# Kernel tuning notes

Measured on AMD Instinct MI355X. Metric: run time of the kernel, lower is better.

Reference implementation:

```python
import jax, jax.numpy as jnp
import numpy as np

NUM_LAYER = 5
EMB = 300
FEAT = 512
NUM_GRAPHS = 64
BN_EPS = 1e-5


def setup_inputs() -> dict:
    key = jax.random.key(0)
    ks = jax.random.split(key, 32)
    N, E = 16000, 256000
    x = jax.random.randint(ks[0], (N, 2), 0, 3)  # col0: atom type (<119), col1: chirality (<3)
    edge_index = jax.random.randint(ks[1], (2, E), 0, N)
    edge_attr = jax.random.randint(ks[2], (E, 2), 0, 3)  # col0: bond type (<6), col1: direction (<3)
    batch = jnp.sort(jax.random.randint(ks[3], (N,), 0, NUM_GRAPHS))

    def xav(k, shape):
        fan_in, fan_out = shape[-2], shape[-1]
        lim = float(np.sqrt(6.0 / (fan_in + fan_out)))
        return jax.random.uniform(k, shape, jnp.float32, -lim, lim)

    inp = dict(x=x, edge_index=edge_index, edge_attr=edge_attr, batch=batch)
    inp['x_emb1'] = xav(ks[4], (119, EMB))
    inp['x_emb2'] = xav(ks[5], (3, EMB))
    inp['e1_emb'] = xav(ks[6], (NUM_LAYER, 6, EMB))
    inp['e2_emb'] = xav(ks[7], (NUM_LAYER, 3, EMB))
    inp['w1'] = xav(ks[8], (NUM_LAYER, EMB, 2 * EMB))
    inp['b1'] = jnp.zeros((NUM_LAYER, 2 * EMB))
    inp['w2'] = xav(ks[9], (NUM_LAYER, 2 * EMB, EMB))
    inp['b2'] = jnp.zeros((NUM_LAYER, EMB))
    inp['bn_g'] = jnp.ones((NUM_LAYER, EMB))
    inp['bn_b'] = jnp.zeros((NUM_LAYER, EMB))
    inp['feat_w'] = xav(ks[10], (EMB, FEAT))
    inp['feat_b'] = jnp.zeros((FEAT,))
    inp['hw1'] = xav(ks[11], (FEAT, FEAT // 2))
    inp['hb1'] = jnp.zeros((FEAT // 2,))
    inp['hw2'] = xav(ks[12], (FEAT // 2, FEAT // 2))
    inp['hb2'] = jnp.zeros((FEAT // 2,))
    inp['hw3'] = xav(ks[13], (FEAT // 2, 2))
    inp['hb3'] = jnp.zeros((2,))
    return inp


def gin_forward(x, edge_index, edge_attr, batch,
                x_emb1, x_emb2, e1_emb, e2_emb, w1, b1, w2, b2,
                bn_g, bn_b, feat_w, feat_b, hw1, hb1, hw2, hb2, hw3, hb3):
    N = x.shape[0]
    h = x_emb1[x[:, 0]] + x_emb2[x[:, 1]]  # [N, EMB]
    # add self-loops once (same for every layer): attr = (5, 0)
    loops = jnp.broadcast_to(jnp.arange(N)[None, :], (2, N))
    ei = jnp.concatenate([edge_index, loops], axis=1)  # [2, E+N]
    loop_attr = jnp.concatenate([jnp.full((N, 1), 5, edge_attr.dtype),
                                 jnp.zeros((N, 1), edge_attr.dtype)], axis=1)
    ea = jnp.concatenate([edge_attr, loop_attr], axis=0)  # [E+N, 2]
    src, dst = ei[0], ei[1]
    for l in range(NUM_LAYER):
        edge_emb = e1_emb[l][ea[:, 0]] + e2_emb[l][ea[:, 1]]  # [E+N, EMB]
        msg = h[src] + edge_emb
        agg = jax.ops.segment_sum(msg, dst, num_segments=N)  # scatter-add
        h = jax.nn.relu(agg @ w1[l] + b1[l]) @ w2[l] + b2[l]  # GIN MLP update
        mean = jnp.mean(h, axis=0)
        var = jnp.var(h, axis=0)
        h = (h - mean) * jax.lax.rsqrt(var + BN_EPS) * bn_g[l] + bn_b[l]
        if l < NUM_LAYER - 1:
            h = jax.nn.relu(h)
    # global mean pool per graph
    sums = jax.ops.segment_sum(h, batch, num_segments=NUM_GRAPHS)
    cnts = jax.ops.segment_sum(jnp.ones((N,), h.dtype), batch, num_segments=NUM_GRAPHS)
    hg = sums / jnp.maximum(cnts, 1.0)[:, None]  # [G, EMB]
    hf = hg @ feat_w + feat_b  # [G, FEAT]
    p = jax.nn.softplus(hf @ hw1 + hb1)
    p = jax.nn.softplus(p @ hw2 + hb2)
    pred = p @ hw3 + hb3  # [G, 2]
    return hf, pred


def reference(x, edge_index, edge_attr, batch,
              x_emb1, x_emb2, e1_emb, e2_emb, w1, b1, w2, b2,
              bn_g, bn_b, feat_w, feat_b, hw1, hb1, hw2, hb2, hw3, hb3):
    return gin_forward(x, edge_index, edge_attr, batch,
                       x_emb1, x_emb2, e1_emb, e2_emb, w1, b1, w2, b2,
                       bn_g, bn_b, feat_w, feat_b, hw1, hb1, hw2, hb2, hw3, hb3)
```

## Files before the change

### kernel.cpp

```cpp
#include <hip/hip_runtime.h>

#define NODES 16000
#define EDGES 256000
#define EMB   300
#define KP1   320
#define NP1   640
#define NP2B  384
#define NGRAPH 64
#define LAYERS 5
#define INV_N (1.0f / 16000.0f)

typedef unsigned short u16;
typedef unsigned int u32;
typedef __bf16 bf16_t;
typedef bf16_t bf16x8 __attribute__((ext_vector_type(8)));
typedef float f32x4 __attribute__((ext_vector_type(4)));

__device__ inline u16 f2bf(float f) {
    bf16_t b = (bf16_t)f;
    return __builtin_bit_cast(u16, b);
}
__device__ inline float bf_lo(u32 u) { return __builtin_bit_cast(float, u << 16); }
__device__ inline float bf_hi(u32 u) { return __builtin_bit_cast(float, u & 0xFFFF0000u); }
__device__ inline u32 bf_pack(float lo, float hi) {
    return ((u32)f2bf(hi) << 16) | (u32)f2bf(lo);
}

__device__ inline float softplus_f(float x) {
    return fmaxf(x, 0.f) + log1pf(expf(-fabsf(x)));
}

__device__ inline void gload_lds16(const u16* g, u16* l) {
    __builtin_amdgcn_global_load_lds(
        (const __attribute__((address_space(1))) void*)g,
        (__attribute__((address_space(3))) void*)l, 16, 0, 0);
}

__device__ inline void bn_coef_v(float ss, float qq, float gg, float bb,
                                 float& s, float& t) {
    float mean = ss * INV_N;
    float var = qq * INV_N - mean * mean;
    float rstd = rsqrtf(var + 1e-5f);
    s = rstd * gg;
    t = bb - mean * s;
}

__global__ void k_count(const int* __restrict__ ei, int* __restrict__ cnt) {
    int e = blockIdx.x * 256 + threadIdx.x;
    if (e >= EDGES) return;
    atomicAdd(&cnt[ei[EDGES + e]], 1);
}

__global__ __launch_bounds__(1024) void k_scan(const int* __restrict__ cnt,
                                               int* __restrict__ row_off,
                                               int* __restrict__ cursor) {
    __shared__ int wsum[16];
    int t = threadIdx.x;
    int lane = t & 63, w = t >> 6;
    int base = t * 16;
    int pre[16];
    int run = 0;
#pragma unroll
    for (int i = 0; i < 16; ++i) {
        int idx = base + i;
        int v = (idx < NODES) ? cnt[idx] : 0;
        pre[i] = run;
        run += v;
    }
    int inc = run;
#pragma unroll
    for (int off = 1; off < 64; off <<= 1) {
        int n = __shfl_up(inc, off);
        if (lane >= off) inc += n;
    }
    if (lane == 63) wsum[w] = inc;
    __syncthreads();
    int wpre = 0;
    for (int i = 0; i < w; ++i) wpre += wsum[i];
    int excl = wpre + inc - run;
#pragma unroll
    for (int i = 0; i < 16; ++i) {
        int idx = base + i;
        if (idx < NODES) {
            int st = excl + pre[i];
            row_off[idx] = st;
            cursor[idx] = st;
        }
    }
    if (t == 1023) row_off[NODES] = wpre + inc;
}

__global__ void k_fill(const int* __restrict__ ei, const int* __restrict__ ea,
                       int* __restrict__ cursor, int* __restrict__ packed) {
    int e = blockIdx.x * 256 + threadIdx.x;
    if (e >= EDGES) return;
    int src = ei[e];
    int dst = ei[EDGES + e];
    int c = ea[e * 2] * 3 + ea[e * 2 + 1];
    int pos = atomicAdd(&cursor[dst], 1);
    packed[pos] = src | (c << 20);
}

#define SEG0 1200000
#define SEG1 6750
#define SEG2 256000
#define SEG3 307200
#define SETUP_TOT (SEG0 + SEG1 + SEG2 + SEG3 + NGRAPH + 1)

__global__ __launch_bounds__(256) void k_setup(
    const int* __restrict__ x, const float* __restrict__ e1x,
    const float* __restrict__ e2x, const float* __restrict__ ce1,
    const float* __restrict__ ce2, const float* __restrict__ w1,
    const float* __restrict__ w2, const int* __restrict__ batch,
    u16* __restrict__ h, u16* __restrict__ comb,
    u16* __restrict__ w1bT, u16* __restrict__ w2bT, int* __restrict__ goff) {
    int id = blockIdx.x * 256 + threadIdx.x;
    if (id < SEG0) {
        int base = id * 4;
        int row = base / EMB;
        int f = base - row * EMB;
        int x1 = x[2 * row], x2 = x[2 * row + 1];
        float4 a = *(const float4*)(e1x + x1 * EMB + f);
        float4 b = *(const float4*)(e2x + x2 * EMB + f);
        u32* o = (u32*)h + id * 2;
        o[0] = bf_pack(a.x + b.x, a.y + b.y);
        o[1] = bf_pack(a.z + b.z, a.w + b.w);
        return;
    }
    id -= SEG0;
    if (id < SEG1) {
        int l = id / 1350, r = id - l * 1350;
        int c = r / 75, f = (r - c * 75) * 4;
        int a = c / 3, bb = c - a * 3;
        float4 va = *(const float4*)(ce1 + (l * 6 + a) * EMB + f);
        float4 vb = *(const float4*)(ce2 + (l * 3 + bb) * EMB + f);
        u32* o = (u32*)comb + ((l * 18 + c) * EMB + f) / 2;
        o[0] = bf_pack(va.x + vb.x, va.y + vb.y);
        o[1] = bf_pack(va.z + vb.z, va.w + vb.w);
        return;
    }
    id -= SEG1;
    if (id < SEG2) {
        int l = id / (NP1 * 80), r = id - l * (NP1 * 80);
        int n = r / 80, k4 = (r - n * 80) * 4;
        float v[4];
#pragma unroll
        for (int j = 0; j < 4; ++j) {
            int k = k4 + j;
            v[j] = (n < 600 && k < EMB) ? w1[(l * EMB + k) * 600 + n] : 0.f;
        }
        u32* o = (u32*)w1bT + ((size_t)(l * NP1 + n) * KP1 + k4) / 2;
        o[0] = bf_pack(v[0], v[1]);
        o[1] = bf_pack(v[2], v[3]);
        return;
    }
    id -= SEG2;
    if (id < SEG3) {
        int l = id / (NP2B * 160), r = id - l * (NP2B * 160);
        int n = r / 160, k4 = (r - n * 160) * 4;
        float v[4];
#pragma unroll
        for (int j = 0; j < 4; ++j) {
            int k = k4 + j;
            v[j] = (n < EMB && k < 600) ? w2[(l * 600 + k) * EMB + n] : 0.f;
        }
        u32* o = (u32*)w2bT + ((size_t)(l * NP2B + n) * NP1 + k4) / 2;
        o[0] = bf_pack(v[0], v[1]);
        o[1] = bf_pack(v[2], v[3]);
        return;
    }
    id -= SEG3;
    if (id <= NGRAPH) {
        int lo = 0, hi = NODES;
        while (lo < hi) { int mid = (lo + hi) >> 1; if (batch[mid] < id) lo = mid + 1; else hi = mid; }
        goff[id] = lo;
    }
}

__global__ __launch_bounds__(256) void k_bnrelu(
    const u16* __restrict__ hin, u16* __restrict__ hout,
    const float* __restrict__ ssum, const float* __restrict__ ssq,
    const float* __restrict__ g, const float* __restrict__ b) {
    int id = blockIdx.x * 256 + threadIdx.x;
    if (id >= NODES * EMB / 4) return;
    int base = id * 4;
    int row = base / EMB;
    int f = base - row * EMB;
    float4 S = *(const float4*)(ssum + f);
    float4 Q = *(const float4*)(ssq + f);
    float4 G = *(const float4*)(g + f);
    float4 B = *(const float4*)(b + f);
    const u32* in = (const u32*)hin + id * 2;
    u32 x0 = in[0], x1 = in[1];
    float sc0, tc0, sc1, tc1, sc2, tc2, sc3, tc3;
    bn_coef_v(S.x, Q.x, G.x, B.x, sc0, tc0);
    bn_coef_v(S.y, Q.y, G.y, B.y, sc1, tc1);
    bn_coef_v(S.z, Q.z, G.z, B.z, sc2, tc2);
    bn_coef_v(S.w, Q.w, G.w, B.w, sc3, tc3);
    float v0 = fmaxf(bf_lo(x0) * sc0 + tc0, 0.f);
    float v1 = fmaxf(bf_hi(x0) * sc1 + tc1, 0.f);
    float v2 = fmaxf(bf_lo(x1) * sc2 + tc2, 0.f);
    float v3 = fmaxf(bf_hi(x1) * sc3 + tc3, 0.f);
    u32* o = (u32*)hout + id * 2;
    o[0] = bf_pack(v0, v1);
    o[1] = bf_pack(v2, v3);
}

#define AGG_E(Q)                                                \
    {                                                           \
        const u32* hr = hu + (size_t)((Q) & 0xFFFFF) * 150;     \
        const u32* cr = cu + ((Q) >> 20) * 150;                 \
        u32 u0 = hr[lane], u1 = hr[64 + lane];                  \
        u32 v0 = cr[lane], v1 = cr[64 + lane];                  \
        u32 u2 = 0, v2 = 0;                                     \
        if (has2) { u2 = hr[128 + lane]; v2 = cr[128 + lane]; } \
        a0l += bf_lo(u0) + bf_lo(v0);                           \
        a0h += bf_hi(u0) + bf_hi(v0);                           \
        a1l += bf_lo(u1) + bf_lo(v1);                           \
        a1h += bf_hi(u1) + bf_hi(v1);                           \
        a2l += bf_lo(u2) + bf_lo(v2);                           \
        a2h += bf_hi(u2) + bf_hi(v2);                           \
    }

__global__ __launch_bounds__(256) void k_aggregate(
    const u16* __restrict__ h, const int* __restrict__ row_off,
    const int* __restrict__ packed, const u16* __restrict__ comb,
    u16* __restrict__ aggB) {
    int node = blockIdx.x * 4 + (threadIdx.x >> 6);
    int lane = threadIdx.x & 63;
    int s = row_off[node], e = row_off[node + 1];
    bool has2 = lane < 22;
    const u32* hu = (const u32*)h;
    const u32* cu = (const u32*)comb;
    float a0l = 0, a0h = 0, a1l = 0, a1h = 0, a2l = 0, a2h = 0;
    {
        const u32* hr = hu + (size_t)node * 150;
        const u32* cr = cu + 15 * 150;
        u32 u0 = hr[lane], u1 = hr[64 + lane];
        u32 v0 = cr[lane], v1 = cr[64 + lane];
        u32 u2 = 0, v2 = 0;
        if (has2) { u2 = hr[128 + lane]; v2 = cr[128 + lane]; }
        a0l = bf_lo(u0) + bf_lo(v0);
        a0h = bf_hi(u0) + bf_hi(v0);
        a1l = bf_lo(u1) + bf_lo(v1);
        a1h = bf_hi(u1) + bf_hi(v1);
        a2l = bf_lo(u2) + bf_lo(v2);
        a2h = bf_hi(u2) + bf_hi(v2);
    }
    int p = s;
    for (; p + 3 < e; p += 4) {
        int q0 = __builtin_amdgcn_readfirstlane(packed[p]);
        int q1 = __builtin_amdgcn_readfirstlane(packed[p + 1]);
        int q2 = __builtin_amdgcn_readfirstlane(packed[p + 2]);
        int q3 = __builtin_amdgcn_readfirstlane(packed[p + 3]);
        AGG_E(q0); AGG_E(q1); AGG_E(q2); AGG_E(q3);
    }
    for (; p < e; ++p) {
        int q = __builtin_amdgcn_readfirstlane(packed[p]);
        AGG_E(q);
    }
    u32* o = (u32*)(aggB + (size_t)node * KP1);
    o[lane] = bf_pack(a0l, a0h);
    o[64 + lane] = bf_pack(a1l, a1h);
    if (lane < 32) o[128 + lane] = has2 ? bf_pack(a2l, a2h) : 0u;
}

template <int MODE>
__global__ __launch_bounds__(256) void k_gemm(
    const u16* __restrict__ A, const u16* __restrict__ Bt,
    const float* __restrict__ bias, int nbias,
    u16* __restrict__ Cv, int ldc, int K,
    float* __restrict__ ssum, float* __restrict__ ssq) {
    __shared__ __align__(16) u16 Al[128 * 32];
    __shared__ __align__(16) u16 Bl[128 * 32];
    __shared__ float rs[2][128];
    __shared__ float rq[2][128];
    int t = threadIdx.x;
    int n0 = blockIdx.x * 128, m0 = blockIdx.y * 128;
    int lane = t & 63, w = t >> 6;
    int wr = w >> 1, wc = w & 1;
    int lr = lane >> 2, lc = lane & 3;
    const u16* gA0 = A + (size_t)(m0 + w * 32 + lr) * K + lc * 8;
    const u16* gA1 = gA0 + (size_t)16 * K;
    const u16* gB0 = Bt + (size_t)(n0 + w * 32 + lr) * K + lc * 8;
    const u16* gB1 = gB0 + (size_t)16 * K;
    u16* lA0 = &Al[(w * 32) * 32];
    u16* lA1 = &Al[(w * 32 + 16) * 32];
    u16* lB0 = &Bl[(w * 32) * 32];
    u16* lB1 = &Bl[(w * 32 + 16) * 32];
    f32x4 acc[4][4];
#pragma unroll
    for (int i = 0; i < 4; i++)
#pragma unroll
        for (int j = 0; j < 4; j++) acc[i][j] = (f32x4){0.f, 0.f, 0.f, 0.f};
    int fr = lane & 15;
    int k0 = (lane >> 4) * 8;
    int abase = (wr * 64 + fr) * 32 + k0;
    int bbase = (wc * 64 + fr) * 32 + k0;
    for (int kt = 0; kt < K; kt += 32) {
        if (kt) __syncthreads();
        gload_lds16(gA0 + kt, lA0);
        gload_lds16(gA1 + kt, lA1);
        gload_lds16(gB0 + kt, lB0);
        gload_lds16(gB1 + kt, lB1);
        __syncthreads();
        bf16x8 af[4], bfv[4];
#pragma unroll
        for (int f = 0; f < 4; ++f) {
            af[f]  = *reinterpret_cast<const bf16x8*>(&Al[abase + f * 16 * 32]);
            bfv[f] = *reinterpret_cast<const bf16x8*>(&Bl[bbase + f * 16 * 32]);
        }
#pragma unroll
        for (int fm = 0; fm < 4; ++fm)
#pragma unroll
            for (int fn = 0; fn < 4; ++fn)
                acc[fm][fn] = __builtin_amdgcn_mfma_f32_16x16x32_bf16(
                    af[fm], bfv[fn], acc[fm][fn], 0, 0, 0);
    }
    int rg = lane >> 4;
    if (MODE == 0) {
#pragma unroll
        for (int fn = 0; fn < 4; ++fn) {
            int col = n0 + wc * 64 + fn * 16 + fr;
            float bv = (col < nbias) ? bias[col] : 0.f;
#pragma unroll
            for (int fm = 0; fm < 4; ++fm) {
                int rb = m0 + wr * 64 + fm * 16 + rg * 4;
#pragma unroll
                for (int j = 0; j < 4; ++j) {
                    float v = fmaxf(acc[fm][fn][j] + bv, 0.f);
                    Cv[(size_t)(rb + j) * ldc + col] = f2bf(v);
                }
            }
        }
    } else {
#pragma unroll
        for (int fn = 0; fn < 4; ++fn) {
            int col = n0 + wc * 64 + fn * 16 + fr;
            float bv = (col < nbias) ? bias[col] : 0.f;
            float cs = 0.f, cq = 0.f;
#pragma unroll
            for (int fm = 0; fm < 4; ++fm) {
                int rb = m0 + wr * 64 + fm * 16 + rg * 4;
#pragma unroll
                for (int j = 0; j < 4; ++j) {
                    float v = acc[fm][fn][j] + bv;
                    if (col < EMB) Cv[(size_t)(rb + j) * EMB + col] = f2bf(v);
                    cs += v;
                    cq += v * v;
                }
            }
            cs += __shfl_xor(cs, 16); cs += __shfl_xor(cs, 32);
            cq += __shfl_xor(cq, 16); cq += __shfl_xor(cq, 32);
            if (rg == 0) {
                rs[wr][wc * 64 + fn * 16 + fr] = cs;
                rq[wr][wc * 64 + fn * 16 + fr] = cq;
            }
        }
        __syncthreads();
        if (t < 128) {
            int col = n0 + t;
            if (col < EMB) {
                atomicAdd(&ssum[col], rs[0][t] + rs[1][t]);
                atomicAdd(&ssq[col], rq[0][t] + rq[1][t]);
            }
        }
    }
}

__global__ __launch_bounds__(256) void k_pool(const u16* __restrict__ h,
                                              const int* __restrict__ goff,
                                              const float* __restrict__ ssum,
                                              const float* __restrict__ ssq,
                                              const float* __restrict__ bng,
                                              const float* __restrict__ bnb,
                                              float* __restrict__ hg) {
    __shared__ float red[4][64];
    int g = blockIdx.x;
    int col = blockIdx.y * 64 + (threadIdx.x & 63);
    int w = threadIdx.x >> 6;
    int s = goff[g], e = goff[g + 1];
    float a = 0.f;
    bool ok = col < EMB;
    if (ok) {
        for (int r = s + w; r < e; r += 4)
            a += __builtin_bit_cast(float, (u32)h[(size_t)r * EMB + col] << 16);
    }
    red[w][threadIdx.x & 63] = a;
    __syncthreads();
    if (w == 0 && ok) {
        float sc, tc;
        bn_coef_v(ssum[col], ssq[col], bng[col], bnb[col], sc, tc);
        float v = red[0][threadIdx.x] + red[1][threadIdx.x] +
                  red[2][threadIdx.x] + red[3][threadIdx.x];
        float inv = (e > s) ? 1.0f / (float)(e - s) : 0.f;
        hg[(size_t)g * EMB + col] = (v * inv) * sc + tc;
    }
}

template <int ACT>
__global__ __launch_bounds__(256) void k_small_mm(
    const float* __restrict__ A, const float* __restrict__ W,
    const float* __restrict__ bias, float* __restrict__ C, int N, int K) {
    __shared__ float red[4][64];
    int row = blockIdx.x;
    int lane = threadIdx.x & 63;
    int col = blockIdx.y * 64 + lane;
    int w = threadIdx.x >> 6;
    const float* a = A + (size_t)row * K;
    float acc = 0.f;
#pragma unroll 4
    for (int k = w; k < K; k += 4) acc += a[k] * W[(size_t)k * N + col];
    red[w][lane] = acc;
    __syncthreads();
    if (w == 0) {
        float v = red[0][lane] + red[1][lane] + red[2][lane] + red[3][lane] + bias[col];
        if (ACT) v = softplus_f(v);
        C[(size_t)row * N + col] = v;
    }
}

__global__ __launch_bounds__(256) void k_pred(const float* __restrict__ P,
                                              const float* __restrict__ hw3,
                                              const float* __restrict__ hb3,
                                              float* __restrict__ out) {
    __shared__ float red[2][4];
    int g = blockIdx.x;
    int t = threadIdx.x;
    float q = P[(size_t)g * 256 + t];
    float r0 = q * hw3[t * 2 + 0];
    float r1 = q * hw3[t * 2 + 1];
#pragma unroll
    for (int off = 32; off > 0; off >>= 1) {
        r0 += __shfl_down(r0, off);
        r1 += __shfl_down(r1, off);
    }
    if ((t & 63) == 0) { red[0][t >> 6] = r0; red[1][t >> 6] = r1; }
    __syncthreads();
    if (t == 0) {
        out[(size_t)NGRAPH * 512 + g * 2 + 0] = red[0][0] + red[0][1] + red[0][2] + red[0][3] + hb3[0];
        out[(size_t)NGRAPH * 512 + g * 2 + 1] = red[1][0] + red[1][1] + red[1][2] + red[1][3] + hb3[1];
    }
}

extern "C" void kernel_launch(void* const* d_in, const int* in_sizes, int n_in,
                              void* d_out, int out_size, void* d_ws, size_t ws_size,
                              hipStream_t stream) {
    const int* x      = (const int*)d_in[0];
    const int* ei     = (const int*)d_in[1];
    const int* ea     = (const int*)d_in[2];
    const int* batch  = (const int*)d_in[3];
    const float* x_emb1 = (const float*)d_in[4];
    const float* x_emb2 = (const float*)d_in[5];
    const float* e1_emb = (const float*)d_in[6];
    const float* e2_emb = (const float*)d_in[7];
    const float* w1   = (const float*)d_in[8];
    const float* b1   = (const float*)d_in[9];
    const float* w2   = (const float*)d_in[10];
    const float* b2   = (const float*)d_in[11];
    const float* bn_g = (const float*)d_in[12];
    const float* bn_b = (const float*)d_in[13];
    const float* feat_w = (const float*)d_in[14];
    const float* feat_b = (const float*)d_in[15];
    const float* hw1  = (const float*)d_in[16];
    const float* hb1  = (const float*)d_in[17];
    const float* hw2  = (const float*)d_in[18];
    const float* hb2  = (const float*)d_in[19];
    const float* hw3  = (const float*)d_in[20];
    const float* hb3  = (const float*)d_in[21];
    float* out = (float*)d_out;

    char* p = (char*)d_ws;
    auto alloc = [&](size_t bytes) -> char* {
        char* r = p;
        p += ((bytes + 255) / 256) * 256;
        return r;
    };
    u16* h_a     = (u16*)alloc((size_t)NODES * EMB * 2);
    u16* h_b     = (u16*)alloc((size_t)NODES * EMB * 2);
    u16* aggB    = (u16*)alloc((size_t)NODES * KP1 * 2);
    u16* T       = (u16*)alloc((size_t)NODES * NP1 * 2);
    u16* w1bT    = (u16*)alloc((size_t)LAYERS * NP1 * KP1 * 2);
    u16* w2bT    = (u16*)alloc((size_t)LAYERS * NP2B * NP1 * 2);
    u16* comb    = (u16*)alloc((size_t)LAYERS * 18 * EMB * 2);
    int* row_off = (int*)alloc((NODES + 1) * 4);
    int* packed  = (int*)alloc((size_t)EDGES * 4);
    int* goff    = (int*)alloc((NGRAPH + 1) * 4);
    float* hg    = (float*)alloc((size_t)NGRAPH * EMB * 4);
    float* pb1   = (float*)alloc((size_t)NGRAPH * 256 * 4);
    float* pb2   = (float*)alloc((size_t)NGRAPH * 256 * 4);
    int* cursor  = (int*)alloc(NODES * 4);
    float* stats5 = (float*)alloc((size_t)LAYERS * 640 * 4);
    if ((size_t)(p - (char*)d_ws) > ws_size) return;

    hipMemsetAsync(cursor, 0, NODES * 4 + LAYERS * 640 * 4, stream);

    k_count<<<(EDGES + 255) / 256, 256, 0, stream>>>(ei, cursor);
    k_scan<<<1, 1024, 0, stream>>>(cursor, row_off, cursor);
    k_fill<<<(EDGES + 255) / 256, 256, 0, stream>>>(ei, ea, cursor, packed);

    k_setup<<<(SETUP_TOT + 255) / 256, 256, 0, stream>>>(
        x, x_emb1, x_emb2, e1_emb, e2_emb, w1, w2, batch,
        h_a, comb, w1bT, w2bT, goff);

    for (int l = 0; l < LAYERS; ++l) {
        const u16* h_src;
        if (l == 0) {
            h_src = h_a;
        } else {
            float* st = stats5 + (size_t)(l - 1) * 640;
            k_bnrelu<<<(NODES * EMB / 4 + 255) / 256, 256, 0, stream>>>(
                h_a, h_b, st, st + 320, bn_g + (l - 1) * EMB, bn_b + (l - 1) * EMB);
            h_src = h_b;
        }
        k_aggregate<<<NODES / 4, 256, 0, stream>>>(
            h_src, row_off, packed, comb + (size_t)l * 18 * EMB, aggB);
        k_gemm<0><<<dim3(NP1 / 128, NODES / 128), 256, 0, stream>>>(
            aggB, w1bT + (size_t)l * NP1 * KP1, b1 + l * 600, 600, T, NP1, KP1,
            nullptr, nullptr);
        float* st = stats5 + (size_t)l * 640;
        k_gemm<1><<<dim3(NP2B / 128, NODES / 128), 256, 0, stream>>>(
            T, w2bT + (size_t)l * NP2B * NP1, b2 + l * EMB, EMB, h_a, 0, NP1,
            st, st + 320);
    }

    float* st4 = stats5 + (size_t)4 * 640;
    k_pool<<<dim3(NGRAPH, 5), 256, 0, stream>>>(h_a, goff, st4, st4 + 320,
                                                bn_g + 4 * EMB, bn_b + 4 * EMB, hg);
    k_small_mm<0><<<dim3(NGRAPH, 8), 256, 0, stream>>>(hg, feat_w, feat_b, out, 512, EMB);
    k_small_mm<1><<<dim3(NGRAPH, 4), 256, 0, stream>>>(out, hw1, hb1, pb1, 256, 512);
    k_small_mm<1><<<dim3(NGRAPH, 4), 256, 0, stream>>>(pb1, hw2, hb2, pb2, 256, 256);
    k_pred<<<NGRAPH, 256, 0, stream>>>(pb2, hw3, hb3, out);
}
```

Measured before the change: 463.7 us.

## Factor edge-embedding sums into per-node bond-type counts in aggregation

k_fill now also builds a per-node histogram over the 18 edge-attribute combos. k_aggregate then gathers only neighbour features per edge and adds each combo embedding once, scaled by its count, instead of loading a combo row for every edge. The feature gathers and the output store also use 8-byte vector loads and stores. This roughly halves the per-edge global reads, at the cost of an extra atomic per edge in setup and 18 count reads per node.

```diff
diff --git a/kernel.cpp b/kernel.cpp
--- a/kernel.cpp
+++ b/kernel.cpp
@@ -91,7 +91,8 @@
 }
 
 __global__ void k_fill(const int* __restrict__ ei, const int* __restrict__ ea,
-                       int* __restrict__ cursor, int* __restrict__ packed) {
+                       int* __restrict__ cursor, int* __restrict__ packed,
+                       int* __restrict__ cnt18) {
     int e = blockIdx.x * 256 + threadIdx.x;
     if (e >= EDGES) return;
     int src = ei[e];
@@ -99,6 +100,7 @@
     int c = ea[e * 2] * 3 + ea[e * 2 + 1];
     int pos = atomicAdd(&cursor[dst], 1);
     packed[pos] = src | (c << 20);
+    atomicAdd(&cnt18[dst * 18 + c], 1);
 }
 
 #define SEG0 1200000
@@ -209,23 +211,18 @@
 #define AGG_E(Q)                                                \
     {                                                           \
         const u32* hr = hu + (size_t)((Q) & 0xFFFFF) * 150;     \
-        const u32* cr = cu + ((Q) >> 20) * 150;                 \
-        u32 u0 = hr[lane], u1 = hr[64 + lane];                  \
-        u32 v0 = cr[lane], v1 = cr[64 + lane];                  \
-        u32 u2 = 0, v2 = 0;                                     \
-        if (has2) { u2 = hr[128 + lane]; v2 = cr[128 + lane]; } \
-        a0l += bf_lo(u0) + bf_lo(v0);                           \
-        a0h += bf_hi(u0) + bf_hi(v0);                           \
-        a1l += bf_lo(u1) + bf_lo(v1);                           \
-        a1h += bf_hi(u1) + bf_hi(v1);                           \
-        a2l += bf_lo(u2) + bf_lo(v2);                           \
-        a2h += bf_hi(u2) + bf_hi(v2);                           \
+        uint2 u01 = *(const uint2*)(hr + 2 * lane);             \
+        u32 u2 = 0;                                             \
+        if (has2) u2 = hr[128 + lane];                          \
+        a0l += bf_lo(u01.x); a0h += bf_hi(u01.x);               \
+        a1l += bf_lo(u01.y); a1h += bf_hi(u01.y);               \
+        a2l += bf_lo(u2);    a2h += bf_hi(u2);                  \
     }
 
 __global__ __launch_bounds__(256) void k_aggregate(
     const u16* __restrict__ h, const int* __restrict__ row_off,
     const int* __restrict__ packed, const u16* __restrict__ comb,
-    u16* __restrict__ aggB) {
+    const int* __restrict__ cnt18, u16* __restrict__ aggB) {
     int node = blockIdx.x * 4 + (threadIdx.x >> 6);
     int lane = threadIdx.x & 63;
     int s = row_off[node], e = row_off[node + 1];
@@ -235,17 +232,12 @@
     float a0l = 0, a0h = 0, a1l = 0, a1h = 0, a2l = 0, a2h = 0;
     {
         const u32* hr = hu + (size_t)node * 150;
-        const u32* cr = cu + 15 * 150;
-        u32 u0 = hr[lane], u1 = hr[64 + lane];
-        u32 v0 = cr[lane], v1 = cr[64 + lane];
-        u32 u2 = 0, v2 = 0;
-        if (has2) { u2 = hr[128 + lane]; v2 = cr[128 + lane]; }
-        a0l = bf_lo(u0) + bf_lo(v0);
-        a0h = bf_hi(u0) + bf_hi(v0);
-        a1l = bf_lo(u1) + bf_lo(v1);
-        a1h = bf_hi(u1) + bf_hi(v1);
-        a2l = bf_lo(u2) + bf_lo(v2);
-        a2h = bf_hi(u2) + bf_hi(v2);
+        uint2 u01 = *(const uint2*)(hr + 2 * lane);
+        u32 u2 = 0;
+        if (has2) u2 = hr[128 + lane];
+        a0l = bf_lo(u01.x); a0h = bf_hi(u01.x);
+        a1l = bf_lo(u01.y); a1h = bf_hi(u01.y);
+        a2l = bf_lo(u2);    a2h = bf_hi(u2);
     }
     int p = s;
     for (; p + 3 < e; p += 4) {
@@ -259,9 +251,26 @@
         int q = __builtin_amdgcn_readfirstlane(packed[p]);
         AGG_E(q);
     }
+    const int* cb = cnt18 + node * 18;
+#pragma unroll
+    for (int c = 0; c < 18; ++c) {
+        int cv = cb[c] + (c == 15 ? 1 : 0);
+        if (cv) {
+            float fc = (float)cv;
+            const u32* cr = cu + c * 150;
+            uint2 v01 = *(const uint2*)(cr + 2 * lane);
+            u32 v2 = 0;
+            if (has2) v2 = cr[128 + lane];
+            a0l += fc * bf_lo(v01.x); a0h += fc * bf_hi(v01.x);
+            a1l += fc * bf_lo(v01.y); a1h += fc * bf_hi(v01.y);
+            a2l += fc * bf_lo(v2);    a2h += fc * bf_hi(v2);
+        }
+    }
     u32* o = (u32*)(aggB + (size_t)node * KP1);
-    o[lane] = bf_pack(a0l, a0h);
-    o[64 + lane] = bf_pack(a1l, a1h);
+    uint2 w01;
+    w01.x = bf_pack(a0l, a0h);
+    w01.y = bf_pack(a1l, a1h);
+    *(uint2*)(o + 2 * lane) = w01;
     if (lane < 32) o[128 + lane] = has2 ? bf_pack(a2l, a2h) : 0u;
 }
 
@@ -489,15 +498,17 @@
     float* hg    = (float*)alloc((size_t)NGRAPH * EMB * 4);
     float* pb1   = (float*)alloc((size_t)NGRAPH * 256 * 4);
     float* pb2   = (float*)alloc((size_t)NGRAPH * 256 * 4);
-    int* cursor  = (int*)alloc(NODES * 4);
+    int* cursor   = (int*)alloc(NODES * 4);
     float* stats5 = (float*)alloc((size_t)LAYERS * 640 * 4);
+    int* cnt18    = (int*)alloc((size_t)NODES * 18 * 4);
     if ((size_t)(p - (char*)d_ws) > ws_size) return;
 
-    hipMemsetAsync(cursor, 0, NODES * 4 + LAYERS * 640 * 4, stream);
+    hipMemsetAsync(cursor, 0, NODES * 4 + LAYERS * 640 * 4 + (size_t)NODES * 18 * 4,
+                   stream);
 
     k_count<<<(EDGES + 255) / 256, 256, 0, stream>>>(ei, cursor);
     k_scan<<<1, 1024, 0, stream>>>(cursor, row_off, cursor);
-    k_fill<<<(EDGES + 255) / 256, 256, 0, stream>>>(ei, ea, cursor, packed);
+    k_fill<<<(EDGES + 255) / 256, 256, 0, stream>>>(ei, ea, cursor, packed, cnt18);
 
     k_setup<<<(SETUP_TOT + 255) / 256, 256, 0, stream>>>(
         x, x_emb1, x_emb2, e1_emb, e2_emb, w1, w2, batch,
@@ -514,7 +525,7 @@
             h_src = h_b;
         }
         k_aggregate<<<NODES / 4, 256, 0, stream>>>(
-            h_src, row_off, packed, comb + (size_t)l * 18 * EMB, aggB);
+            h_src, row_off, packed, comb + (size_t)l * 18 * EMB, cnt18, aggB);
         k_gemm<0><<<dim3(NP1 / 128, NODES / 128), 256, 0, stream>>>(
             aggB, w1bT + (size_t)l * NP1 * KP1, b1 + l * 600, 600, T, NP1, KP1,
             nullptr, nullptr);
```

After: 519.8 us. +12.1%, slower.

## Double-buffer LDS tiles in GEMM to overlap global loads with MFMA

Applied to the files above, without the earlier changes.

Splits the GEMM's A and B shared-memory tiles into two buffers. The next K-slice is prefetched with direct-to-LDS loads while the current slice feeds the MFMA instructions, and one barrier per step replaces two. This aims to hide global load latency behind compute, at the cost of doubled LDS use per block, which may lower occupancy. Correctness depends on the barrier also covering completion of the async LDS loads (vmcnt) before the buffer is read.

```diff
diff --git a/kernel.cpp b/kernel.cpp
--- a/kernel.cpp
+++ b/kernel.cpp
@@ -271,8 +271,8 @@
     const float* __restrict__ bias, int nbias,
     u16* __restrict__ Cv, int ldc, int K,
     float* __restrict__ ssum, float* __restrict__ ssq) {
-    __shared__ __align__(16) u16 Al[128 * 32];
-    __shared__ __align__(16) u16 Bl[128 * 32];
+    __shared__ __align__(16) u16 Al[2][128 * 32];
+    __shared__ __align__(16) u16 Bl[2][128 * 32];
     __shared__ float rs[2][128];
     __shared__ float rq[2][128];
     int t = threadIdx.x;
@@ -284,10 +284,8 @@
     const u16* gA1 = gA0 + (size_t)16 * K;
     const u16* gB0 = Bt + (size_t)(n0 + w * 32 + lr) * K + lc * 8;
     const u16* gB1 = gB0 + (size_t)16 * K;
-    u16* lA0 = &Al[(w * 32) * 32];
-    u16* lA1 = &Al[(w * 32 + 16) * 32];
-    u16* lB0 = &Bl[(w * 32) * 32];
-    u16* lB1 = &Bl[(w * 32 + 16) * 32];
+    int lds0 = (w * 32) * 32;
+    int lds1 = (w * 32 + 16) * 32;
     f32x4 acc[4][4];
 #pragma unroll
     for (int i = 0; i < 4; i++)
@@ -297,18 +295,26 @@
     int k0 = (lane >> 4) * 8;
     int abase = (wr * 64 + fr) * 32 + k0;
     int bbase = (wc * 64 + fr) * 32 + k0;
-    for (int kt = 0; kt < K; kt += 32) {
-        if (kt) __syncthreads();
-        gload_lds16(gA0 + kt, lA0);
-        gload_lds16(gA1 + kt, lA1);
-        gload_lds16(gB0 + kt, lB0);
-        gload_lds16(gB1 + kt, lB1);
-        __syncthreads();
+    int nsteps = K >> 5;
+    gload_lds16(gA0, &Al[0][lds0]);
+    gload_lds16(gA1, &Al[0][lds1]);
+    gload_lds16(gB0, &Bl[0][lds0]);
+    gload_lds16(gB1, &Bl[0][lds1]);
+    __syncthreads();
+    int cur = 0;
+    for (int s = 0; s < nsteps; ++s) {
+        if (s + 1 < nsteps) {
+            int kt = (s + 1) << 5;
+            gload_lds16(gA0 + kt, &Al[cur ^ 1][lds0]);
+            gload_lds16(gA1 + kt, &Al[cur ^ 1][lds1]);
+            gload_lds16(gB0 + kt, &Bl[cur ^ 1][lds0]);
+            gload_lds16(gB1 + kt, &Bl[cur ^ 1][lds1]);
+        }
         bf16x8 af[4], bfv[4];
 #pragma unroll
         for (int f = 0; f < 4; ++f) {
-            af[f]  = *reinterpret_cast<const bf16x8*>(&Al[abase + f * 16 * 32]);
-            bfv[f] = *reinterpret_cast<const bf16x8*>(&Bl[bbase + f * 16 * 32]);
+            af[f]  = *reinterpret_cast<const bf16x8*>(&Al[cur][abase + f * 16 * 32]);
+            bfv[f] = *reinterpret_cast<const bf16x8*>(&Bl[cur][bbase + f * 16 * 32]);
         }
 #pragma unroll
         for (int fm = 0; fm < 4; ++fm)
@@ -316,6 +322,10 @@
             for (int fn = 0; fn < 4; ++fn)
                 acc[fm][fn] = __builtin_amdgcn_mfma_f32_16x16x32_bf16(
                     af[fm], bfv[fn], acc[fm][fn], 0, 0, 0);
+        if (s + 1 < nsteps) {
+            __syncthreads();
+            cur ^= 1;
+        }
     }
     int rg = lane >> 4;
     if (MODE == 0) {
```

New measurement: 465.4 us. No clear change (+0.4%).
